# Optimization experiments

Hardware: AMD Instinct MI355X
Metric: run time of the kernel (lower is better)

Reference implementation:

```python
import jax, jax.numpy as jnp
import numpy as np

D_MODEL = 1024
N_HEADS = 16
HEAD_DIM = D_MODEL // N_HEADS
ROPE_BASE = 10000.0


def rotate_half(x):
    x1, x2 = x[..., : x.shape[-1] // 2], x[..., x.shape[-1] // 2 :]
    return jnp.concatenate((-x2, x1), axis=-1)


def rope_cos_sin(L, dim, dtype):
    inv_freq = 1.0 / (ROPE_BASE ** (jnp.arange(0, dim, 2, dtype=jnp.float32) / dim))
    freqs = jnp.arange(L, dtype=jnp.float32)[:, None] * inv_freq[None, :]  # [L, dim/2]
    emb = jnp.concatenate((freqs, freqs), axis=-1)  # [L, dim]
    # broadcast over batch and heads: [1, L, 1, dim]
    return jnp.cos(emb)[None, :, None, :].astype(dtype), jnp.sin(emb)[None, :, None, :].astype(dtype)


def setup_inputs() -> dict:
    key = jax.random.key(0)
    ks = jax.random.split(key, 11)
    N, L, S = 2, 2048, 2048
    s = 1.0 / np.sqrt(D_MODEL)
    return {
        "queries": jax.random.normal(ks[0], (N, L, D_MODEL), jnp.float32),
        "keys": jax.random.normal(ks[1], (N, S, D_MODEL), jnp.float32),
        "values": jax.random.normal(ks[2], (N, S, D_MODEL), jnp.float32),
        "Wq": jax.random.normal(ks[3], (D_MODEL, D_MODEL), jnp.float32) * s,
        "bq": jnp.zeros((D_MODEL,), jnp.float32),
        "Wk": jax.random.normal(ks[4], (D_MODEL, D_MODEL), jnp.float32) * s,
        "bk": jnp.zeros((D_MODEL,), jnp.float32),
        "Wv": jax.random.normal(ks[5], (D_MODEL, D_MODEL), jnp.float32) * s,
        "bv": jnp.zeros((D_MODEL,), jnp.float32),
        "Wo": jax.random.normal(ks[6], (D_MODEL, D_MODEL), jnp.float32) * s,
        "bo": jnp.zeros((D_MODEL,), jnp.float32),
    }


def reference(queries, keys, values, Wq, bq, Wk, bk, Wv, bv, Wo, bo):
    N, L, _ = queries.shape
    S = keys.shape[1]
    H, hd = N_HEADS, HEAD_DIM

    # QKV projections (nn.Linear: x @ W.T + b), reshape to [N, T, H, hd]
    q = (jnp.einsum("nld,ed->nle", queries, Wq) + bq).reshape(N, L, H, hd)
    k = (jnp.einsum("nsd,ed->nse", keys, Wk) + bk).reshape(N, S, H, hd)
    v = (jnp.einsum("nsd,ed->nse", values, Wv) + bv).reshape(N, S, H, hd)

    # Rotary embedding: q*cos + rotate_half(q)*sin  (same for k)
    cos, sin = rope_cos_sin(L, hd, q.dtype)
    q = q * cos + rotate_half(q) * sin
    k = k * cos + rotate_half(k) * sin

    # Inner attention: scaled dot-product with causal mask
    scores = jnp.einsum("nlhd,nshd->nhls", q, k) / jnp.sqrt(jnp.asarray(hd, q.dtype))
    causal = jnp.tril(jnp.ones((L, S), bool))
    scores = jnp.where(causal[None, None], scores, jnp.asarray(-1e9, scores.dtype))
    attn = jax.nn.softmax(scores, axis=-1)
    out = jnp.einsum("nhls,nshd->nlhd", attn, v).reshape(N, L, H * hd)

    # Output projection
    return jnp.einsum("nle,de->nld", out, Wo) + bo
```

## Files before the change

### kernel.cpp

```cpp
#include <hip/hip_runtime.h>
#include <math.h>

#define DM 1024
#define NH 16
#define HD 64
#define SEQ 2048
#define NB2 2
#define MROWS 4096

typedef unsigned short u16;
typedef __attribute__((ext_vector_type(8))) short short8;
typedef __attribute__((ext_vector_type(4))) float f32x4;
typedef __attribute__((ext_vector_type(2))) unsigned int u32x2;

#define GLOAD16(g, l) __builtin_amdgcn_global_load_lds( \
    (const __attribute__((address_space(1))) void*)(g),  \
    (__attribute__((address_space(3))) void*)(l), 16, 0, 0)

static __device__ __forceinline__ u16 f2bf(float f) {
  union { float f; unsigned u; } v; v.f = f;
  unsigned r = v.u + 0x7fffu + ((v.u >> 16) & 1u);
  return (u16)(r >> 16);
}

static __device__ __forceinline__ short8 cvt8(float4 a, float4 b) {
  short8 s;
  s[0] = (short)f2bf(a.x); s[1] = (short)f2bf(a.y);
  s[2] = (short)f2bf(a.z); s[3] = (short)f2bf(a.w);
  s[4] = (short)f2bf(b.x); s[5] = (short)f2bf(b.y);
  s[6] = (short)f2bf(b.z); s[7] = (short)f2bf(b.w);
  return s;
}

__global__ void conv_all(
    const float* __restrict__ q, const float* __restrict__ k, const float* __restrict__ v,
    const float* __restrict__ wq, const float* __restrict__ wk,
    const float* __restrict__ wv, const float* __restrict__ wo,
    u16* __restrict__ xq, u16* __restrict__ xk, u16* __restrict__ xv,
    u16* __restrict__ wqb, u16* __restrict__ wkb, u16* __restrict__ wvb, u16* __restrict__ wob,
    float* __restrict__ cosT, float* __restrict__ sinT)
{
  const int z = blockIdx.z;
  const int idx = blockIdx.x * blockDim.x + threadIdx.x;
  if (z == 7) {
    if (idx >= SEQ * 32) return;
    int l = idx >> 5, i = idx & 31;
    float invf = expf(-(float)i * (9.210340371976184f / 32.0f));
    float ang = (float)l * invf;
    float s, c;
    sincosf(ang, &s, &c);
    cosT[idx] = c; sinT[idx] = s;
    return;
  }
  const float* src; u16* dst; int n;
  switch (z) {
    case 0: src = q;  dst = xq;  n = MROWS * DM; break;
    case 1: src = k;  dst = xk;  n = MROWS * DM; break;
    case 2: src = v;  dst = xv;  n = MROWS * DM; break;
    case 3: src = wq; dst = wqb; n = DM * DM; break;
    case 4: src = wk; dst = wkb; n = DM * DM; break;
    case 5: src = wv; dst = wvb; n = DM * DM; break;
    default: src = wo; dst = wob; n = DM * DM; break;
  }
  const int base = idx * 8;
  if (base >= n) return;
  float4 a = *(const float4*)(src + base);
  float4 b = *(const float4*)(src + base + 4);
  *(short8*)(dst + base) = cvt8(a, b);
}

__global__ __launch_bounds__(512) void gemm_qkv(
    const u16* __restrict__ Xq, const u16* __restrict__ Xk, const u16* __restrict__ Xv,
    const u16* __restrict__ Wqb, const u16* __restrict__ Wkb, const u16* __restrict__ Wvb,
    const float* __restrict__ bq, const float* __restrict__ bk, const float* __restrict__ bv,
    u16* __restrict__ Qb, u16* __restrict__ Kb, u16* __restrict__ VT,
    const float* __restrict__ cosT, const float* __restrict__ sinT)
{
  __shared__ __align__(16) u16 SH[49152];
  const int z = blockIdx.z;
  const u16* A = (z == 0) ? Xq : (z == 1) ? Xk : Xv;
  const u16* W = (z == 0) ? Wqb : (z == 1) ? Wkb : Wvb;
  const float* bias = (z == 0) ? bq : (z == 1) ? bk : bv;
  const int row0 = blockIdx.x * 256, col0 = blockIdx.y * 256;

  const int tid = threadIdx.x;
  const int lane = tid & 63;
  const int wid = tid >> 6;
  const int wm = wid >> 2;
  const int wn = wid & 3;
  const int fr = lane & 15, kg = lane >> 4;

  const u16* ga = A + (size_t)(row0 + (tid & 255)) * DM + ((tid >> 8) << 3);
  const u16* gb = W + (size_t)(col0 + (tid & 255)) * DM + ((tid >> 8) << 3);
  const int lw = (wid >> 2) * 2048 + (wid & 3) * 512;
  u16* B0 = SH;
  u16* B1 = SH + 16384;
  u16* B2 = SH + 32768;

  f32x4 acc[8][4];
#pragma unroll
  for (int m = 0; m < 8; ++m)
#pragma unroll
    for (int n = 0; n < 4; ++n) acc[m][n] = (f32x4){0.f, 0.f, 0.f, 0.f};

  auto issueA = [&](int t, u16* buf) {
    const int ko = t * 32;
    GLOAD16(ga + ko, buf + lw);
    GLOAD16(ga + ko + 16, buf + lw + 4096);
  };
  auto issueB = [&](int t, u16* buf) {
    const int ko = t * 32;
    GLOAD16(gb + ko, buf + 8192 + lw);
    GLOAD16(gb + ko + 16, buf + 8192 + lw + 4096);
  };

  auto phA = [&](const u16* bufR, u16* bufW, int t2, short8* bfr) {
    short8 afr[4];
#pragma unroll
    for (int m = 0; m < 4; ++m)
      afr[m] = *(const short8*)(&bufR[kg * 2048 + (wm * 128 + m * 16 + fr) * 8]);
#pragma unroll
    for (int n = 0; n < 4; ++n)
      bfr[n] = *(const short8*)(&bufR[8192 + kg * 2048 + (wn * 64 + n * 16 + fr) * 8]);
    if (t2 < 32) issueA(t2, bufW);
    __builtin_amdgcn_sched_barrier(0);
    __builtin_amdgcn_s_barrier();
    __builtin_amdgcn_sched_barrier(0);
    __builtin_amdgcn_s_setprio(1);
#pragma unroll
    for (int m = 0; m < 4; ++m)
#pragma unroll
      for (int n = 0; n < 4; ++n)
        acc[m][n] = __builtin_amdgcn_mfma_f32_16x16x32_bf16(afr[m], bfr[n], acc[m][n], 0, 0, 0);
    __builtin_amdgcn_s_setprio(0);
    __builtin_amdgcn_sched_barrier(0);
    __builtin_amdgcn_s_barrier();
    __builtin_amdgcn_sched_barrier(0);
  };
  auto phB = [&](const u16* bufR, u16* bufW, int t2, const short8* bfr) {
    short8 afr[4];
#pragma unroll
    for (int m = 0; m < 4; ++m)
      afr[m] = *(const short8*)(&bufR[kg * 2048 + (wm * 128 + (m + 4) * 16 + fr) * 8]);
    if (t2 < 32) issueB(t2, bufW);
    __builtin_amdgcn_sched_barrier(0);
    __builtin_amdgcn_s_barrier();
    __builtin_amdgcn_sched_barrier(0);
    __builtin_amdgcn_s_setprio(1);
#pragma unroll
    for (int m = 0; m < 4; ++m)
#pragma unroll
      for (int n = 0; n < 4; ++n)
        acc[m + 4][n] = __builtin_amdgcn_mfma_f32_16x16x32_bf16(afr[m], bfr[n], acc[m + 4][n], 0, 0, 0);
    __builtin_amdgcn_s_setprio(0);
  };

  issueA(0, B0); issueB(0, B0);
  issueA(1, B1); issueB(1, B1);

#define QSTEP(WLIT, bufR, bufW, t2) do {                            \
    asm volatile("s_waitcnt vmcnt(" WLIT ")" ::: "memory");         \
    __builtin_amdgcn_sched_barrier(0);                              \
    __builtin_amdgcn_s_barrier();                                   \
    __builtin_amdgcn_sched_barrier(0);                              \
    short8 bfr[4];                                                  \
    phA(bufR, bufW, t2, bfr);                                       \
    phB(bufR, bufW, t2, bfr);                                       \
  } while (0)

  for (int t = 0; t < 30; t += 3) {
    QSTEP("4", B0, B2, t + 2);
    QSTEP("4", B1, B0, t + 3);
    QSTEP("4", B2, B1, t + 4);
  }
  QSTEP("4", B0, B2, 32);
  QSTEP("0", B1, B2, 33);
#undef QSTEP

  if (z == 2) {
    __syncthreads();
    const int nb = row0 >> 11;
    const int sbase = row0 & (SEQ - 1);
#pragma unroll
    for (int p = 0; p < 4; ++p) {
      if (wn == p) {
#pragma unroll
        for (int n = 0; n < 4; ++n) {
          const int dcol = n * 16 + fr;
          const float bv = bias[col0 + p * 64 + dcol];
#pragma unroll
          for (int m = 0; m < 8; ++m)
#pragma unroll
            for (int r = 0; r < 4; ++r)
              SH[dcol * 264 + wm * 128 + m * 16 + kg * 4 + r] = f2bf(acc[m][n][r] + bv);
        }
      }
      __syncthreads();
      {
        const int dcol = tid >> 3, sq = tid & 7;
        const int e = col0 + p * 64 + dcol;
        u16* dst = VT + ((size_t)(nb * NH + (e >> 6)) * HD + (e & 63)) * SEQ + sbase + sq * 32;
#pragma unroll
        for (int j = 0; j < 4; ++j)
          *(short8*)(dst + j * 8) = *(const short8*)(&SH[dcol * 264 + sq * 32 + j * 8]);
      }
      __syncthreads();
    }
    return;
  }

  const float qscale = (z == 0) ? 0.125f : 1.0f;
  u16* Cb = (z == 0) ? Qb : Kb;
#pragma unroll
  for (int m = 0; m < 8; ++m) {
#pragma unroll
    for (int r = 0; r < 4; ++r) {
      const int rowg = row0 + wm * 128 + m * 16 + kg * 4 + r;
      const int l = rowg & (SEQ - 1);
#pragma unroll
      for (int n = 0; n < 4; ++n) {
        const int colg = col0 + wn * 64 + n * 16 + fr;
        const int i = n * 16 + fr;
        const int fi = i & 31;
        const float c = cosT[l * 32 + fi];
        const float s = sinT[l * 32 + fi];
        const float v = acc[m][n][r] + bias[colg];
        const float pv = acc[m][n ^ 2][r] + bias[col0 + wn * 64 + ((n ^ 2) * 16 + fr)];
        const float o = v * c + ((i < 32) ? -pv : pv) * s;
        Cb[(size_t)rowg * DM + colg] = f2bf(o * qscale);
      }
    }
  }
}

__global__ __launch_bounds__(256) void gemm_o(
    const u16* __restrict__ Ob, const u16* __restrict__ Wob,
    const float* __restrict__ bo, float* __restrict__ out)
{
  __shared__ __align__(16) u16 SH[24576];
  const int row0 = blockIdx.x * 128, col0 = blockIdx.y * 128;
  const int tid = threadIdx.x;
  const int lane = tid & 63;
  const int w = tid >> 6;
  const int wr = w >> 1;
  const int wc = w & 1;
  const int fr = lane & 15, kg = lane >> 4;

  const u16* ga = Ob + (size_t)(row0 + (tid & 127)) * DM + ((tid >> 7) << 3);
  const u16* gb = Wob + (size_t)(col0 + (tid & 127)) * DM + ((tid >> 7) << 3);
  const int lw = w * 512;
  u16* B0 = SH;
  u16* B1 = SH + 8192;
  u16* B2 = SH + 16384;

  f32x4 acc[4][4];
#pragma unroll
  for (int m = 0; m < 4; ++m)
#pragma unroll
    for (int n = 0; n < 4; ++n) acc[m][n] = (f32x4){0.f, 0.f, 0.f, 0.f};

  auto issueA = [&](int t, u16* buf) {
    const int ko = t * 32;
    GLOAD16(ga + ko, buf + lw);
    GLOAD16(ga + ko + 16, buf + lw + 2048);
  };
  auto issueB = [&](int t, u16* buf) {
    const int ko = t * 32;
    GLOAD16(gb + ko, buf + 4096 + lw);
    GLOAD16(gb + ko + 16, buf + 4096 + lw + 2048);
  };

  auto phA = [&](const u16* bufR, u16* bufW, int t2, short8* bfr) {
    short8 afr[2];
#pragma unroll
    for (int m = 0; m < 2; ++m)
      afr[m] = *(const short8*)(&bufR[kg * 1024 + (wr * 64 + m * 16 + fr) * 8]);
#pragma unroll
    for (int n = 0; n < 4; ++n)
      bfr[n] = *(const short8*)(&bufR[4096 + kg * 1024 + (wc * 64 + n * 16 + fr) * 8]);
    if (t2 < 32) issueA(t2, bufW);
    __builtin_amdgcn_sched_barrier(0);
    __builtin_amdgcn_s_barrier();
    __builtin_amdgcn_sched_barrier(0);
    __builtin_amdgcn_s_setprio(1);
#pragma unroll
    for (int m = 0; m < 2; ++m)
#pragma unroll
      for (int n = 0; n < 4; ++n)
        acc[m][n] = __builtin_amdgcn_mfma_f32_16x16x32_bf16(afr[m], bfr[n], acc[m][n], 0, 0, 0);
    __builtin_amdgcn_s_setprio(0);
    __builtin_amdgcn_sched_barrier(0);
    __builtin_amdgcn_s_barrier();
    __builtin_amdgcn_sched_barrier(0);
  };
  auto phB = [&](const u16* bufR, u16* bufW, int t2, const short8* bfr) {
    short8 afr[2];
#pragma unroll
    for (int m = 0; m < 2; ++m)
      afr[m] = *(const short8*)(&bufR[kg * 1024 + (wr * 64 + (m + 2) * 16 + fr) * 8]);
    if (t2 < 32) issueB(t2, bufW);
    __builtin_amdgcn_sched_barrier(0);
    __builtin_amdgcn_s_barrier();
    __builtin_amdgcn_sched_barrier(0);
    __builtin_amdgcn_s_setprio(1);
#pragma unroll
    for (int m = 0; m < 2; ++m)
#pragma unroll
      for (int n = 0; n < 4; ++n)
        acc[m + 2][n] = __builtin_amdgcn_mfma_f32_16x16x32_bf16(afr[m], bfr[n], acc[m + 2][n], 0, 0, 0);
    __builtin_amdgcn_s_setprio(0);
  };

  issueA(0, B0); issueB(0, B0);
  issueA(1, B1); issueB(1, B1);

#define OSTEP(WLIT, bufR, bufW, t2) do {                            \
    asm volatile("s_waitcnt vmcnt(" WLIT ")" ::: "memory");         \
    __builtin_amdgcn_sched_barrier(0);                              \
    __builtin_amdgcn_s_barrier();                                   \
    __builtin_amdgcn_sched_barrier(0);                              \
    short8 bfr[4];                                                  \
    phA(bufR, bufW, t2, bfr);                                       \
    phB(bufR, bufW, t2, bfr);                                       \
  } while (0)

  for (int t = 0; t < 30; t += 3) {
    OSTEP("4", B0, B2, t + 2);
    OSTEP("4", B1, B0, t + 3);
    OSTEP("4", B2, B1, t + 4);
  }
  OSTEP("4", B0, B2, 32);
  OSTEP("0", B1, B2, 33);
#undef OSTEP

#pragma unroll
  for (int m = 0; m < 4; ++m) {
#pragma unroll
    for (int r = 0; r < 4; ++r) {
      const int rowg = row0 + wr * 64 + m * 16 + kg * 4 + r;
#pragma unroll
      for (int n = 0; n < 4; ++n) {
        const int colg = col0 + wc * 64 + n * 16 + fr;
        out[(size_t)rowg * DM + colg] = acc[m][n][r] + bo[colg];
      }
    }
  }
}

__global__ __launch_bounds__(512) void flash_attn(
    const u16* __restrict__ Qp, const u16* __restrict__ Kp,
    const u16* __restrict__ VT, u16* __restrict__ Op)
{
  __shared__ __align__(16) u16 Ks[4096];
  __shared__ __align__(16) u16 Vt[4096];
  __shared__ __align__(16) u16 Pl[9216];

  const int tid = threadIdx.x;
  const int lane = tid & 63;
  const int w = tid >> 6;
  const int fr = lane & 15, rg = lane >> 4;
  const int qbp = blockIdx.x;
  const int h = blockIdx.y, nb = blockIdx.z;

  const size_t headoff = (size_t)nb * SEQ * DM + (size_t)h * HD;
  const size_t vthead = (size_t)(nb * NH + h) * HD * SEQ;
  const int srow = tid >> 3;
  const int sch  = tid & 7;
  u16* Pw = &Pl[w * 1152];

  for (int pass = 0; pass < 2; ++pass) {
    const int qe = pass ? (15 - qbp) : qbp;
    const int KBend = 2 * qe + 2;
    const int qrow0 = qe * 128 + w * 16;
    const int qg = qrow0 + fr;

    short8 qf[2];
#pragma unroll
    for (int ck = 0; ck < 2; ++ck)
      qf[ck] = *(const short8*)(Qp + headoff + (size_t)(qrow0 + fr) * DM + ck * 32 + rg * 8);

    f32x4 accO[4];
#pragma unroll
    for (int df = 0; df < 4; ++df) accO[df] = (f32x4){0.f, 0.f, 0.f, 0.f};
    float m_run = -3e38f, l_run = 0.f;

    short8 kpf = *(const short8*)(Kp + headoff + (size_t)srow * DM + sch * 8);
    short8 vpf = *(const short8*)(VT + vthead + (size_t)srow * SEQ + sch * 8);

    for (int kb = 0; kb < KBend; ++kb) {
      *(short8*)(&Ks[(sch * 64 + (srow ^ sch)) * 8]) = kpf;
      *(short8*)(&Vt[(sch * 64 + (srow ^ sch)) * 8]) = vpf;
      __syncthreads();
      if (kb + 1 < KBend) {
        kpf = *(const short8*)(Kp + headoff + (size_t)((kb + 1) * 64 + srow) * DM + sch * 8);
        vpf = *(const short8*)(VT + vthead + (size_t)srow * SEQ + (kb + 1) * 64 + sch * 8);
      }

      const bool active = (kb * 64) <= (qrow0 + 15);
      if (active) {
        short8 kf[4][2];
#pragma unroll
        for (int sf = 0; sf < 4; ++sf)
#pragma unroll
          for (int ck = 0; ck < 2; ++ck) {
            const int dc = ck * 4 + rg;
            kf[sf][ck] = *(const short8*)(&Ks[(dc * 64 + ((sf * 16 + fr) ^ dc)) * 8]);
          }
        f32x4 sc_[4];
#pragma unroll
        for (int sf = 0; sf < 4; ++sf) {
          f32x4 z = (f32x4){0.f, 0.f, 0.f, 0.f};
#pragma unroll
          for (int ck = 0; ck < 2; ++ck)
            z = __builtin_amdgcn_mfma_f32_16x16x32_bf16(kf[sf][ck], qf[ck], z, 0, 0, 0);
          sc_[sf] = z;
        }
        float rowmax = -3e38f;
#pragma unroll
        for (int sf = 0; sf < 4; ++sf)
#pragma unroll
          for (int r = 0; r < 4; ++r) {
            const int sg = kb * 64 + sf * 16 + rg * 4 + r;
            float v = sc_[sf][r];
            v = (sg <= qg) ? v : -3e38f;
            sc_[sf][r] = v;
            rowmax = fmaxf(rowmax, v);
          }
        rowmax = fmaxf(rowmax, __shfl_xor(rowmax, 16, 64));
        rowmax = fmaxf(rowmax, __shfl_xor(rowmax, 32, 64));
        const float mnew = fmaxf(m_run, rowmax);
        const float scl = __expf(m_run - mnew);
        m_run = mnew;
        float psum = 0.f;
#pragma unroll
        for (int sf = 0; sf < 4; ++sf)
#pragma unroll
          for (int r = 0; r < 4; ++r) {
            const float p = __expf(sc_[sf][r] - mnew);
            sc_[sf][r] = p;
            psum += p;
          }
        psum += __shfl_xor(psum, 16, 64);
        psum += __shfl_xor(psum, 32, 64);
        l_run = l_run * scl + psum;
        const float s0 = __shfl(scl, rg * 4 + 0, 64);
        const float s1 = __shfl(scl, rg * 4 + 1, 64);
        const float s2 = __shfl(scl, rg * 4 + 2, 64);
        const float s3 = __shfl(scl, rg * 4 + 3, 64);
#pragma unroll
        for (int df = 0; df < 4; ++df) {
          accO[df][0] *= s0; accO[df][1] *= s1;
          accO[df][2] *= s2; accO[df][3] *= s3;
        }
#pragma unroll
        for (int sf = 0; sf < 4; ++sf) {
          u32x2 pv;
          pv[0] = (unsigned)f2bf(sc_[sf][0]) | ((unsigned)f2bf(sc_[sf][1]) << 16);
          pv[1] = (unsigned)f2bf(sc_[sf][2]) | ((unsigned)f2bf(sc_[sf][3]) << 16);
          *(u32x2*)(&Pw[fr * 72 + (sf * 8 + rg * 2) * 2]) = pv;
        }
        short8 pa[2];
#pragma unroll
        for (int ck = 0; ck < 2; ++ck)
          pa[ck] = *(const short8*)(&Pw[fr * 72 + (ck * 16 + rg * 4) * 2]);
#pragma unroll
        for (int df = 0; df < 4; ++df)
#pragma unroll
          for (int ck = 0; ck < 2; ++ck) {
            const int sc = ck * 4 + rg;
            const short8 vf = *(const short8*)(&Vt[(sc * 64 + ((df * 16 + fr) ^ sc)) * 8]);
            accO[df] = __builtin_amdgcn_mfma_f32_16x16x32_bf16(pa[ck], vf, accO[df], 0, 0, 0);
          }
      }
      __syncthreads();
    }

    const float l0 = __shfl(l_run, rg * 4 + 0, 64);
    const float l1 = __shfl(l_run, rg * 4 + 1, 64);
    const float l2 = __shfl(l_run, rg * 4 + 2, 64);
    const float l3 = __shfl(l_run, rg * 4 + 3, 64);
#pragma unroll
    for (int df = 0; df < 4; ++df) {
      const int d = df * 16 + fr;
      Op[headoff + (size_t)(qrow0 + rg * 4 + 0) * DM + d] = f2bf(accO[df][0] / l0);
      Op[headoff + (size_t)(qrow0 + rg * 4 + 1) * DM + d] = f2bf(accO[df][1] / l1);
      Op[headoff + (size_t)(qrow0 + rg * 4 + 2) * DM + d] = f2bf(accO[df][2] / l2);
      Op[headoff + (size_t)(qrow0 + rg * 4 + 3) * DM + d] = f2bf(accO[df][3] / l3);
    }
  }
}

extern "C" void kernel_launch(void* const* d_in, const int* in_sizes, int n_in,
                              void* d_out, int out_size, void* d_ws, size_t ws_size,
                              hipStream_t stream) {
  (void)in_sizes; (void)n_in; (void)out_size; (void)ws_size;
  const float* queries = (const float*)d_in[0];
  const float* keys    = (const float*)d_in[1];
  const float* values  = (const float*)d_in[2];
  const float* Wq = (const float*)d_in[3];
  const float* bq = (const float*)d_in[4];
  const float* Wk = (const float*)d_in[5];
  const float* bk = (const float*)d_in[6];
  const float* Wv = (const float*)d_in[7];
  const float* bv = (const float*)d_in[8];
  const float* Wo = (const float*)d_in[9];
  const float* bo = (const float*)d_in[10];
  float* out = (float*)d_out;

  char* ws = (char*)d_ws;
  const size_t MB = 1u << 20;
  u16* Qb  = (u16*)(ws);
  u16* Kb  = (u16*)(ws + 8 * MB);
  u16* VTg = (u16*)(ws + 16 * MB);
  u16* Xq  = (u16*)(ws + 24 * MB);
  u16* Ob  = Xq;
  u16* Xk  = (u16*)(ws + 32 * MB);
  u16* Xv  = (u16*)(ws + 40 * MB);
  u16* Wqb = (u16*)(ws + 48 * MB);
  u16* Wkb = (u16*)(ws + 50 * MB);
  u16* Wvb = (u16*)(ws + 52 * MB);
  u16* Wob = (u16*)(ws + 54 * MB);
  float* cosT = (float*)(ws + 56 * MB);
  float* sinT = (float*)(ws + 56 * MB + 256 * 1024);

  conv_all<<<dim3(2048, 1, 8), 256, 0, stream>>>(
      queries, keys, values, Wq, Wk, Wv, Wo,
      Xq, Xk, Xv, Wqb, Wkb, Wvb, Wob, cosT, sinT);
  gemm_qkv<<<dim3(MROWS / 256, DM / 256, 3), 512, 0, stream>>>(
      Xq, Xk, Xv, Wqb, Wkb, Wvb, bq, bk, bv, Qb, Kb, VTg, cosT, sinT);
  flash_attn<<<dim3(SEQ / 256, NH, NB2), 512, 0, stream>>>(Qb, Kb, VTg, Ob);
  gemm_o<<<dim3(MROWS / 128, DM / 128), 512 / 2, 0, stream>>>(Ob, Wob, bo, out);
}
```

Baseline: 142.1 us.

## Fuse fp32-to-bf16 activation conversion into QKV GEMM A-tile loading

The separate pass that converted the query/key/value activations to bf16 is removed. The QKV GEMM now loads fp32 activation tiles into registers, converts them, and writes bf16 into LDS inside its software pipeline, while weights still use async global-to-LDS loads. This avoids writing and re-reading about 24 MB of bf16 intermediates. In exchange, the GEMM reads twice the bytes per A tile and adds register pressure and VALU conversion work. It also needs extra waits on LDS writes inside the main loop.

```diff
diff --git a/kernel.cpp b/kernel.cpp
--- a/kernel.cpp
+++ b/kernel.cpp
@@ -32,17 +32,15 @@
   return s;
 }
 
-__global__ void conv_all(
-    const float* __restrict__ q, const float* __restrict__ k, const float* __restrict__ v,
+__global__ void conv_w(
     const float* __restrict__ wq, const float* __restrict__ wk,
     const float* __restrict__ wv, const float* __restrict__ wo,
-    u16* __restrict__ xq, u16* __restrict__ xk, u16* __restrict__ xv,
     u16* __restrict__ wqb, u16* __restrict__ wkb, u16* __restrict__ wvb, u16* __restrict__ wob,
     float* __restrict__ cosT, float* __restrict__ sinT)
 {
   const int z = blockIdx.z;
   const int idx = blockIdx.x * blockDim.x + threadIdx.x;
-  if (z == 7) {
+  if (z == 4) {
     if (idx >= SEQ * 32) return;
     int l = idx >> 5, i = idx & 31;
     float invf = expf(-(float)i * (9.210340371976184f / 32.0f));
@@ -52,25 +50,22 @@
     cosT[idx] = c; sinT[idx] = s;
     return;
   }
-  const float* src; u16* dst; int n;
+  const float* src; u16* dst;
   switch (z) {
-    case 0: src = q;  dst = xq;  n = MROWS * DM; break;
-    case 1: src = k;  dst = xk;  n = MROWS * DM; break;
-    case 2: src = v;  dst = xv;  n = MROWS * DM; break;
-    case 3: src = wq; dst = wqb; n = DM * DM; break;
-    case 4: src = wk; dst = wkb; n = DM * DM; break;
-    case 5: src = wv; dst = wvb; n = DM * DM; break;
-    default: src = wo; dst = wob; n = DM * DM; break;
+    case 0: src = wq; dst = wqb; break;
+    case 1: src = wk; dst = wkb; break;
+    case 2: src = wv; dst = wvb; break;
+    default: src = wo; dst = wob; break;
   }
   const int base = idx * 8;
-  if (base >= n) return;
+  if (base >= DM * DM) return;
   float4 a = *(const float4*)(src + base);
   float4 b = *(const float4*)(src + base + 4);
   *(short8*)(dst + base) = cvt8(a, b);
 }
 
 __global__ __launch_bounds__(512) void gemm_qkv(
-    const u16* __restrict__ Xq, const u16* __restrict__ Xk, const u16* __restrict__ Xv,
+    const float* __restrict__ Qf, const float* __restrict__ Kf, const float* __restrict__ Vf,
     const u16* __restrict__ Wqb, const u16* __restrict__ Wkb, const u16* __restrict__ Wvb,
     const float* __restrict__ bq, const float* __restrict__ bk, const float* __restrict__ bv,
     u16* __restrict__ Qb, u16* __restrict__ Kb, u16* __restrict__ VT,
@@ -78,7 +73,7 @@
 {
   __shared__ __align__(16) u16 SH[49152];
   const int z = blockIdx.z;
-  const u16* A = (z == 0) ? Xq : (z == 1) ? Xk : Xv;
+  const float* Af = (z == 0) ? Qf : (z == 1) ? Kf : Vf;
   const u16* W = (z == 0) ? Wqb : (z == 1) ? Wkb : Wvb;
   const float* bias = (z == 0) ? bq : (z == 1) ? bk : bv;
   const int row0 = blockIdx.x * 256, col0 = blockIdx.y * 256;
@@ -89,9 +84,12 @@
   const int wm = wid >> 2;
   const int wn = wid & 3;
   const int fr = lane & 15, kg = lane >> 4;
-
-  const u16* ga = A + (size_t)(row0 + (tid & 255)) * DM + ((tid >> 8) << 3);
-  const u16* gb = W + (size_t)(col0 + (tid & 255)) * DM + ((tid >> 8) << 3);
+  const int row = tid & 255;
+  const int h = tid >> 8;
+  const int rw8 = row * 8;
+
+  const float* gaf = Af + (size_t)(row0 + row) * DM + h * 16;
+  const u16* gb = W + (size_t)(col0 + row) * DM + (h << 3);
   const int lw = (wid >> 2) * 2048 + (wid & 3) * 512;
   u16* B0 = SH;
   u16* B1 = SH + 16384;
@@ -103,10 +101,18 @@
 #pragma unroll
     for (int n = 0; n < 4; ++n) acc[m][n] = (f32x4){0.f, 0.f, 0.f, 0.f};
 
-  auto issueA = [&](int t, u16* buf) {
-    const int ko = t * 32;
-    GLOAD16(ga + ko, buf + lw);
-    GLOAD16(ga + ko + 16, buf + lw + 4096);
+  float4 ar0, ar1, ar2, ar3;
+
+  auto loadA = [&](int t) {
+    const float* g = gaf + (size_t)t * 32;
+    ar0 = *(const float4*)(g);
+    ar1 = *(const float4*)(g + 4);
+    ar2 = *(const float4*)(g + 8);
+    ar3 = *(const float4*)(g + 12);
+  };
+  auto writeA = [&](u16* buf) {
+    *(short8*)(buf + (2 * h) * 2048 + rw8)     = cvt8(ar0, ar1);
+    *(short8*)(buf + (2 * h + 1) * 2048 + rw8) = cvt8(ar2, ar3);
   };
   auto issueB = [&](int t, u16* buf) {
     const int ko = t * 32;
@@ -114,7 +120,7 @@
     GLOAD16(gb + ko + 16, buf + 8192 + lw + 4096);
   };
 
-  auto phA = [&](const u16* bufR, u16* bufW, int t2, short8* bfr) {
+  auto phA = [&](const u16* bufR, int s, short8* bfr) {
     short8 afr[4];
 #pragma unroll
     for (int m = 0; m < 4; ++m)
@@ -122,7 +128,7 @@
 #pragma unroll
     for (int n = 0; n < 4; ++n)
       bfr[n] = *(const short8*)(&bufR[8192 + kg * 2048 + (wn * 64 + n * 16 + fr) * 8]);
-    if (t2 < 32) issueA(t2, bufW);
+    if (s <= 29) loadA(s + 2);
     __builtin_amdgcn_sched_barrier(0);
     __builtin_amdgcn_s_barrier();
     __builtin_amdgcn_sched_barrier(0);
@@ -137,12 +143,12 @@
     __builtin_amdgcn_s_barrier();
     __builtin_amdgcn_sched_barrier(0);
   };
-  auto phB = [&](const u16* bufR, u16* bufW, int t2, const short8* bfr) {
+  auto phB = [&](const u16* bufR, u16* bufWB, int s, const short8* bfr) {
     short8 afr[4];
 #pragma unroll
     for (int m = 0; m < 4; ++m)
       afr[m] = *(const short8*)(&bufR[kg * 2048 + (wm * 128 + (m + 4) * 16 + fr) * 8]);
-    if (t2 < 32) issueB(t2, bufW);
+    if (s <= 29) issueB(s + 2, bufWB);
     __builtin_amdgcn_sched_barrier(0);
     __builtin_amdgcn_s_barrier();
     __builtin_amdgcn_sched_barrier(0);
@@ -155,26 +161,31 @@
     __builtin_amdgcn_s_setprio(0);
   };
 
-  issueA(0, B0); issueB(0, B0);
-  issueA(1, B1); issueB(1, B1);
-
-#define QSTEP(WLIT, bufR, bufW, t2) do {                            \
-    asm volatile("s_waitcnt vmcnt(" WLIT ")" ::: "memory");         \
+  loadA(0);
+  issueB(0, B0);
+  asm volatile("s_waitcnt vmcnt(2)" ::: "memory");
+  writeA(B0);
+  loadA(1);
+  issueB(1, B1);
+
+#define QSTEP(WLIT, bufR, bufWA, bufWB, s) do {                     \
+    asm volatile("s_waitcnt vmcnt(" WLIT ") lgkmcnt(0)" ::: "memory"); \
     __builtin_amdgcn_sched_barrier(0);                              \
     __builtin_amdgcn_s_barrier();                                   \
     __builtin_amdgcn_sched_barrier(0);                              \
+    if ((s) <= 30) writeA(bufWA);                                   \
     short8 bfr[4];                                                  \
-    phA(bufR, bufW, t2, bfr);                                       \
-    phB(bufR, bufW, t2, bfr);                                       \
+    phA(bufR, (s), bfr);                                            \
+    phB(bufR, bufWB, (s), bfr);                                     \
   } while (0)
 
   for (int t = 0; t < 30; t += 3) {
-    QSTEP("4", B0, B2, t + 2);
-    QSTEP("4", B1, B0, t + 3);
-    QSTEP("4", B2, B1, t + 4);
-  }
-  QSTEP("4", B0, B2, 32);
-  QSTEP("0", B1, B2, 33);
+    QSTEP("2", B0, B1, B2, t);
+    QSTEP("2", B1, B2, B0, t + 1);
+    QSTEP("2", B2, B0, B1, t + 2);
+  }
+  QSTEP("2", B0, B1, B2, 30);
+  QSTEP("0", B1, B2, B0, 31);
 #undef QSTEP
 
   if (z == 2) {
@@ -512,10 +523,7 @@
   u16* Qb  = (u16*)(ws);
   u16* Kb  = (u16*)(ws + 8 * MB);
   u16* VTg = (u16*)(ws + 16 * MB);
-  u16* Xq  = (u16*)(ws + 24 * MB);
-  u16* Ob  = Xq;
-  u16* Xk  = (u16*)(ws + 32 * MB);
-  u16* Xv  = (u16*)(ws + 40 * MB);
+  u16* Ob  = (u16*)(ws + 24 * MB);
   u16* Wqb = (u16*)(ws + 48 * MB);
   u16* Wkb = (u16*)(ws + 50 * MB);
   u16* Wvb = (u16*)(ws + 52 * MB);
@@ -523,11 +531,10 @@
   float* cosT = (float*)(ws + 56 * MB);
   float* sinT = (float*)(ws + 56 * MB + 256 * 1024);
 
-  conv_all<<<dim3(2048, 1, 8), 256, 0, stream>>>(
-      queries, keys, values, Wq, Wk, Wv, Wo,
-      Xq, Xk, Xv, Wqb, Wkb, Wvb, Wob, cosT, sinT);
+  conv_w<<<dim3(512, 1, 5), 256, 0, stream>>>(
+      Wq, Wk, Wv, Wo, Wqb, Wkb, Wvb, Wob, cosT, sinT);
   gemm_qkv<<<dim3(MROWS / 256, DM / 256, 3), 512, 0, stream>>>(
-      Xq, Xk, Xv, Wqb, Wkb, Wvb, bq, bk, bv, Qb, Kb, VTg, cosT, sinT);
+      queries, keys, values, Wqb, Wkb, Wvb, bq, bk, bv, Qb, Kb, VTg, cosT, sinT);
   flash_attn<<<dim3(SEQ / 256, NH, NB2), 512, 0, stream>>>(Qb, Kb, VTg, Ob);
-  gemm_o<<<dim3(MROWS / 128, DM / 128), 512 / 2, 0, stream>>>(Ob, Wob, bo, out);
-}
+  gemm_o<<<dim3(MROWS / 128, DM / 128), 256, 0, stream>>>(Ob, Wob, bo, out);
+}
```

New measurement: 151.9 us. +6.9%, slower.
